# Kernel optimization log

Measured on AMD Instinct MI355X. Metric: run time of the kernel, lower is better.

The kernel has to match this reference:

```python
import jax, jax.numpy as jnp
import numpy as np

N = 2_000_000
FUN, TAU, ALPHA, LOSS_WEIGHT = 'log', 1.0, 1.0, 1.0


def setup_inputs() -> dict:
    key = jax.random.key(0)
    k1, k2, k3 = jax.random.split(key, 3)
    pred = jax.random.uniform(k1, (N, 5), dtype=jnp.float32)
    target = jax.random.uniform(k2, (N, 5), dtype=jnp.float32)
    weight = jax.random.uniform(k3, (N,), dtype=jnp.float32)
    return {"pred": pred, "target": target, "weight": weight}


def _xyrs(xywhr):
    # [N,5] -> xy [N,2], R [N,2,2], S [N,2,2] (diag(wh/2))
    xy = xywhr[:, :2]
    wh = xywhr[:, 2:4]
    r = xywhr[:, 4]
    c, s = jnp.cos(r), jnp.sin(r)
    R = jnp.stack([c, -s, s, c], axis=-1).reshape(-1, 2, 2)
    S = 0.5 * wh[:, :, None] * jnp.eye(2, dtype=xywhr.dtype)  # diag_embed
    return xy, R, S


def _sqrt_trace_2x2sym(M):
    # trace of matrix sqrt of symmetric PSD 2x2: sqrt(tr(M) + 2*sqrt(det(M)))
    a, b, d = M[:, 0, 0], M[:, 0, 1], M[:, 1, 1]
    det = jnp.clip(a * d - b * b, 0.0)
    return jnp.sqrt(jnp.clip(a + d + 2.0 * jnp.sqrt(det), 0.0))


def reference(pred, target, weight):
    xy_p, R_p, S_p = _xyrs(pred)
    xy_t, R_t, S_t = _xyrs(target)

    dxy = xy_p - xy_t
    xy_distance = jnp.sum(dxy * dxy, axis=-1)

    Rp_T = jnp.swapaxes(R_p, -1, -2)
    Rt_T = jnp.swapaxes(R_t, -1, -2)
    Sigma_p_sqrt = R_p @ S_p @ Rp_T
    Sigma_p = R_p @ (S_p * S_p) @ Rp_T
    Sigma_t = R_t @ (S_t * S_t) @ Rt_T

    whr_distance = Sigma_p[:, 0, 0] + Sigma_p[:, 1, 1]
    whr_distance = whr_distance + Sigma_t[:, 0, 0] + Sigma_t[:, 1, 1]
    cross = Sigma_p_sqrt @ Sigma_t @ Sigma_p_sqrt
    whr_distance = whr_distance - 2.0 * _sqrt_trace_2x2sym(cross)

    distance = jnp.sqrt(jnp.clip(xy_distance + ALPHA * whr_distance, 0.0))
    scale = jnp.sqrt(jnp.sqrt(jnp.prod(pred[:, 2:4] * target[:, 2:4], axis=-1)))
    distance = distance / scale

    if FUN == 'log':
        distance = jnp.log1p(distance)
    elif FUN == 'sqrt':
        distance = jnp.sqrt(distance)

    if TAU >= 1.0:
        loss = 1.0 - 1.0 / (TAU + distance)
    else:
        loss = distance

    # weighted_loss wrapper: elementwise weight then mean reduction
    loss = jnp.mean(loss * weight)
    return loss * LOSS_WEIGHT
```

## Files before the change

kernel.cpp:

```cpp
#include <hip/hip_runtime.h>


__device__ __forceinline__ float gwd_row(const float* __restrict__ p,
                                         const float* __restrict__ t)
{
    const float px = p[0], py = p[1], pw = p[2], ph = p[3], pr = p[4];
    const float tx = t[0], ty = t[1], tw = t[2], th = t[3], tr = t[4];

    const float dx = px - tx;
    const float dy = py - ty;
    const float xy_dist = dx * dx + dy * dy;

    const float a2p = 0.25f * pw * pw;
    const float b2p = 0.25f * ph * ph;
    const float a2t = 0.25f * tw * tw;
    const float b2t = 0.25f * th * th;

    float whr = (a2p + b2p) + (a2t + b2t);

    float cp, sp, ct, st;
    __sincosf(pr, &sp, &cp);
    __sincosf(tr, &st, &ct);

    const float Sp00 = cp * cp * a2p + sp * sp * b2p;
    const float Sp01 = cp * sp * (a2p - b2p);
    const float Sp11 = sp * sp * a2p + cp * cp * b2p;
    const float St00 = ct * ct * a2t + st * st * b2t;
    const float St01 = ct * st * (a2t - b2t);
    const float St11 = st * st * a2t + ct * ct * b2t;

    const float tr_cross  = Sp00 * St00 + 2.0f * Sp01 * St01 + Sp11 * St11;
    const float det_cross = (a2p * b2p) * (a2t * b2t);

    float sq = fmaxf(tr_cross + 2.0f * sqrtf(det_cross), 0.0f);
    whr = whr - 2.0f * sqrtf(sq);

    float distance = sqrtf(fmaxf(xy_dist + whr, 0.0f));

    const float prod = (pw * tw) * (ph * th);
    distance = distance / sqrtf(sqrtf(prod));

    distance = log1pf(distance);
    return 1.0f - 1.0f / (1.0f + distance);
}

__global__ __launch_bounds__(256) void gwd_loss_kernel(
    const float* __restrict__ pred,
    const float* __restrict__ target,
    const float* __restrict__ weight,
    float* __restrict__ out,
    int n)
{
    const float inv_n = 1.0f / (float)n;
    const int g  = blockIdx.x * 256 + threadIdx.x;
    const int r0 = g * 4;
    float acc = 0.0f;

    if (r0 + 3 < n) {
        const float4* p4 = (const float4*)pred   + (size_t)g * 5;
        const float4* t4 = (const float4*)target + (size_t)g * 5;
        const float4  w4 = ((const float4*)weight)[g];

        float pbuf[20], tbuf[20];
        float4 P0 = p4[0], P1 = p4[1], P2 = p4[2], P3 = p4[3], P4 = p4[4];
        float4 T0 = t4[0], T1 = t4[1], T2 = t4[2], T3 = t4[3], T4 = t4[4];
        *(float4*)(pbuf +  0) = P0; *(float4*)(pbuf +  4) = P1;
        *(float4*)(pbuf +  8) = P2; *(float4*)(pbuf + 12) = P3;
        *(float4*)(pbuf + 16) = P4;
        *(float4*)(tbuf +  0) = T0; *(float4*)(tbuf +  4) = T1;
        *(float4*)(tbuf +  8) = T2; *(float4*)(tbuf + 12) = T3;
        *(float4*)(tbuf + 16) = T4;

        const float w[4] = { w4.x, w4.y, w4.z, w4.w };
        #pragma unroll
        for (int j = 0; j < 4; ++j)
            acc += gwd_row(&pbuf[j * 5], &tbuf[j * 5]) * w[j];
    } else {
        for (int r = r0; r < n && r < r0 + 4; ++r) {
            float pb[5], tb[5];
            #pragma unroll
            for (int k = 0; k < 5; ++k) { pb[k] = pred[r * 5 + k]; tb[k] = target[r * 5 + k]; }
            acc += gwd_row(pb, tb) * weight[r];
        }
    }

    #pragma unroll
    for (int off = 32; off > 0; off >>= 1)
        acc += __shfl_down(acc, off, 64);

    __shared__ float wave_sums[4];
    const int lane = threadIdx.x & 63;
    const int wid  = threadIdx.x >> 6;
    if (lane == 0) wave_sums[wid] = acc;
    __syncthreads();

    if (threadIdx.x == 0) {
        const float s = (wave_sums[0] + wave_sums[1]) + (wave_sums[2] + wave_sums[3]);
        atomicAdd(out, s * inv_n);
    }
}

extern "C" void kernel_launch(void* const* d_in, const int* in_sizes, int n_in,
                              void* d_out, int out_size, void* d_ws, size_t ws_size,
                              hipStream_t stream) {
    const float* pred   = (const float*)d_in[0];
    const float* target = (const float*)d_in[1];
    const float* weight = (const float*)d_in[2];
    float* out = (float*)d_out;

    const int n = in_sizes[2];

    hipMemsetAsync(out, 0, sizeof(float), stream);

    const int block  = 256;
    const int groups = (n + 3) / 4;
    const int grid   = (groups + block - 1) / block;
    gwd_loss_kernel<<<grid, block, 0, stream>>>(pred, target, weight, out, n);
}
```

Measured before the change: 126.1 us.

## Stage pred/target chunks through shared memory with coalesced float4 loads

Each block now loads a 1024-row chunk of pred and target with fully coalesced float4 loads into LDS, then each thread computes four rows from shared memory using strided row indices. Weight reads become coalesced scalar loads. This targets the uncoalesced 80-byte-stride per-thread vector loads of the previous layout, at the cost of 40KB LDS per block, an extra barrier, and lower occupancy.

```diff
diff --git a/kernel.cpp b/kernel.cpp
--- a/kernel.cpp
+++ b/kernel.cpp
@@ -1,5 +1,7 @@
 #include <hip/hip_runtime.h>
 
+
+#define CHUNK_ROWS 1024
 
 __device__ __forceinline__ float gwd_row(const float* __restrict__ p,
                                          const float* __restrict__ t)
@@ -51,35 +53,43 @@
     float* __restrict__ out,
     int n)
 {
+    __shared__ float s_pred[CHUNK_ROWS * 5];
+    __shared__ float s_tgt [CHUNK_ROWS * 5];
+
     const float inv_n = 1.0f / (float)n;
-    const int g  = blockIdx.x * 256 + threadIdx.x;
-    const int r0 = g * 4;
+    const int row0 = blockIdx.x * CHUNK_ROWS;
+    const int tid  = threadIdx.x;
     float acc = 0.0f;
 
-    if (r0 + 3 < n) {
-        const float4* p4 = (const float4*)pred   + (size_t)g * 5;
-        const float4* t4 = (const float4*)target + (size_t)g * 5;
-        const float4  w4 = ((const float4*)weight)[g];
+    if (row0 + CHUNK_ROWS <= n) {
+        const float4* p4 = (const float4*)(pred   + (size_t)row0 * 5);
+        const float4* t4 = (const float4*)(target + (size_t)row0 * 5);
 
-        float pbuf[20], tbuf[20];
-        float4 P0 = p4[0], P1 = p4[1], P2 = p4[2], P3 = p4[3], P4 = p4[4];
-        float4 T0 = t4[0], T1 = t4[1], T2 = t4[2], T3 = t4[3], T4 = t4[4];
-        *(float4*)(pbuf +  0) = P0; *(float4*)(pbuf +  4) = P1;
-        *(float4*)(pbuf +  8) = P2; *(float4*)(pbuf + 12) = P3;
-        *(float4*)(pbuf + 16) = P4;
-        *(float4*)(tbuf +  0) = T0; *(float4*)(tbuf +  4) = T1;
-        *(float4*)(tbuf +  8) = T2; *(float4*)(tbuf + 12) = T3;
-        *(float4*)(tbuf + 16) = T4;
+        float4 P[5], T[5];
+        #pragma unroll
+        for (int j = 0; j < 5; ++j) P[j] = p4[j * 256 + tid];
+        #pragma unroll
+        for (int j = 0; j < 5; ++j) T[j] = t4[j * 256 + tid];
 
-        const float w[4] = { w4.x, w4.y, w4.z, w4.w };
         #pragma unroll
-        for (int j = 0; j < 4; ++j)
-            acc += gwd_row(&pbuf[j * 5], &tbuf[j * 5]) * w[j];
+        for (int j = 0; j < 5; ++j) ((float4*)s_pred)[j * 256 + tid] = P[j];
+        #pragma unroll
+        for (int j = 0; j < 5; ++j) ((float4*)s_tgt )[j * 256 + tid] = T[j];
+        __syncthreads();
+
+        #pragma unroll
+        for (int rr = 0; rr < 4; ++rr) {
+            const int r = tid + rr * 256;
+            acc += gwd_row(&s_pred[r * 5], &s_tgt[r * 5]) * weight[row0 + r];
+        }
     } else {
-        for (int r = r0; r < n && r < r0 + 4; ++r) {
+        for (int r = row0 + tid; r < n; r += 256) {
             float pb[5], tb[5];
             #pragma unroll
-            for (int k = 0; k < 5; ++k) { pb[k] = pred[r * 5 + k]; tb[k] = target[r * 5 + k]; }
+            for (int k = 0; k < 5; ++k) {
+                pb[k] = pred  [(size_t)r * 5 + k];
+                tb[k] = target[(size_t)r * 5 + k];
+            }
             acc += gwd_row(pb, tb) * weight[r];
         }
     }
@@ -88,14 +98,14 @@
     for (int off = 32; off > 0; off >>= 1)
         acc += __shfl_down(acc, off, 64);
 
-    __shared__ float wave_sums[4];
-    const int lane = threadIdx.x & 63;
-    const int wid  = threadIdx.x >> 6;
-    if (lane == 0) wave_sums[wid] = acc;
+    __syncthreads();
+    const int lane = tid & 63;
+    const int wid  = tid >> 6;
+    if (lane == 0) s_pred[wid] = acc;
     __syncthreads();
 
-    if (threadIdx.x == 0) {
-        const float s = (wave_sums[0] + wave_sums[1]) + (wave_sums[2] + wave_sums[3]);
+    if (tid == 0) {
+        const float s = (s_pred[0] + s_pred[1]) + (s_pred[2] + s_pred[3]);
         atomicAdd(out, s * inv_n);
     }
 }
@@ -112,8 +122,7 @@
 
     hipMemsetAsync(out, 0, sizeof(float), stream);
 
-    const int block  = 256;
-    const int groups = (n + 3) / 4;
-    const int grid   = (groups + block - 1) / block;
+    const int block = 256;
+    const int grid  = (n + CHUNK_ROWS - 1) / CHUNK_ROWS;
     gwd_loss_kernel<<<grid, block, 0, stream>>>(pred, target, weight, out, n);
 }
```

After: 125.2 us. No clear change (-0.7%).
